# Kernel optimization log

Hardware: AMD Instinct MI355X
Metric: run time of the kernel (lower is better)

Reference implementation:

```python
import jax, jax.numpy as jnp
import numpy as np

H = 2  # num_heads hardcoded in the torch module


def setup_inputs() -> dict:
    key = jax.random.key(0)
    ks = jax.random.split(key, 10)
    B, S, D = 8, 2048, 512
    s = 0.02
    return {
        "rgb": jax.random.normal(ks[0], (B, S, D), jnp.float32),
        "event": jax.random.normal(ks[1], (B, S, D), jnp.float32),
        "w_rgb": jax.random.normal(ks[2], (D, D), jnp.float32) * s,
        "b_rgb": jnp.zeros((D,), jnp.float32),
        "w_event": jax.random.normal(ks[3], (D, D), jnp.float32) * s,
        "b_event": jnp.zeros((D,), jnp.float32),
        "w_in": jax.random.normal(ks[4], (3 * D, D), jnp.float32) * s,   # packed QKV in_proj, torch layout
        "b_in": jnp.zeros((3 * D,), jnp.float32),
        "w_out": jax.random.normal(ks[5], (D, D), jnp.float32) * s,
        "b_out": jnp.zeros((D,), jnp.float32),
    }


def _mha(q_in, kv_in, w_in, b_in, w_out, b_out):
    """torch nn.MultiheadAttention with key==value==kv_in, batch-first math."""
    B, S, D = q_in.shape
    hd = D // H
    q = q_in @ w_in[:D].T + b_in[:D]
    k = kv_in @ w_in[D:2 * D].T + b_in[D:2 * D]
    v = kv_in @ w_in[2 * D:].T + b_in[2 * D:]
    q = q.reshape(B, S, H, hd) * (1.0 / np.sqrt(hd))
    k = k.reshape(B, S, H, hd)
    v = v.reshape(B, S, H, hd)
    scores = jnp.einsum('bqhd,bkhd->bhqk', q, k)          # [B,H,S,S]
    attn = jax.nn.softmax(scores, axis=-1)
    out = jnp.einsum('bhqk,bkhd->bqhd', attn, v).reshape(B, S, D)
    return out @ w_out.T + b_out


def reference(rgb, event, w_rgb, b_rgb, w_event, b_event, w_in, b_in, w_out, b_out):
    rgb_p = rgb @ w_rgb.T + b_rgb
    event_p = event @ w_event.T + b_event
    # same attention weights used for both cross directions
    event_attn = _mha(rgb_p, event_p, w_in, b_in, w_out, b_out)
    rgb_attn = _mha(event_p, rgb_p, w_in, b_in, w_out, b_out)
    gate = jax.nn.sigmoid(jnp.sum(rgb_p * event_p, axis=-1, keepdims=True))
    fused = gate * event_attn + (1.0 - gate) * rgb_attn
    return fused + (rgb_p + event_p) * 0.5
```

## Files before the change

### kernel.cpp

```cpp
#include <hip/hip_runtime.h>
#include <hip/hip_bf16.h>
#include <stdint.h>


typedef __bf16 bf16_t;
typedef __bf16 bf16x8 __attribute__((ext_vector_type(8)));
typedef float f32x4 __attribute__((ext_vector_type(4)));
typedef float f32x16 __attribute__((ext_vector_type(16)));
typedef unsigned int u32;

typedef void gvoid_t __attribute__((address_space(1)));
typedef void svoid_t __attribute__((address_space(3)));

__device__ inline void gload16(const void* g, void* l) {
    __builtin_amdgcn_global_load_lds((gvoid_t*)g, (svoid_t*)l, 16, 0, 0);
}

__device__ inline u32 cvtpk_bf16(float lo, float hi) {
    u32 r;
    asm("v_cvt_pk_bf16_f32 %0, %1, %2" : "=v"(r) : "v"(lo), "v"(hi));
    return r;
}

__device__ inline float exp2v(float x) {
    float r;
    asm("v_exp_f32 %0, %1" : "=v"(r) : "v"(x));
    return r;
}

__global__ __launch_bounds__(256) void f2b_all(const float* __restrict__ s0, bf16_t* __restrict__ d0,
                                               const float* __restrict__ s1, bf16_t* __restrict__ d1,
                                               const float* __restrict__ s2, bf16_t* __restrict__ d2,
                                               const float* __restrict__ s3, bf16_t* __restrict__ d3,
                                               const float* __restrict__ s4, bf16_t* __restrict__ d4,
                                               const float* __restrict__ s5, bf16_t* __restrict__ d5) {
    int i = blockIdx.x * 256 + threadIdx.x;
    const float* s; bf16_t* d; int off;
    if (i < 1048576)      { s = s0; d = d0; off = i; }
    else if (i < 2097152) { s = s1; d = d1; off = i - 1048576; }
    else if (i < 2129920) { s = s2; d = d2; off = i - 2097152; }
    else if (i < 2162688) { s = s3; d = d3; off = i - 2129920; }
    else if (i < 2260992) { s = s4; d = d4; off = i - 2162688; }
    else                  { s = s5; d = d5; off = i - 2260992; }
    const float4* p = reinterpret_cast<const float4*>(s) + (size_t)off * 2;
    float4 a = p[0], b = p[1];
    bf16x8 o;
    o[0] = (bf16_t)a.x; o[1] = (bf16_t)a.y; o[2] = (bf16_t)a.z; o[3] = (bf16_t)a.w;
    o[4] = (bf16_t)b.x; o[5] = (bf16_t)b.y; o[6] = (bf16_t)b.z; o[7] = (bf16_t)b.w;
    reinterpret_cast<bf16x8*>(d)[off] = o;
}

template <int MODE>
__global__ __launch_bounds__(256) void gemm_bt(const bf16_t* __restrict__ A,
                                               const bf16_t* __restrict__ A2,
                                               const bf16_t* __restrict__ Bw,
                                               const bf16_t* __restrict__ Bw2,
                                               const float* __restrict__ bias,
                                               const float* __restrict__ bias2,
                                               void* __restrict__ Cout,
                                               void* __restrict__ Cout2,
                                               const bf16_t* __restrict__ r1,
                                               const bf16_t* __restrict__ r2,
                                               const float* __restrict__ gate,
                                               bf16_t* __restrict__ qdst,
                                               bf16_t* __restrict__ kdst,
                                               bf16_t* __restrict__ vdst,
                                               bf16_t* __restrict__ qdst2,
                                               bf16_t* __restrict__ kdst2,
                                               bf16_t* __restrict__ vdst2,
                                               int N, int K) {
    __shared__ __align__(16) bf16_t As[128][64];
    __shared__ __align__(16) bf16_t Bs[128][64];
    const int tid = threadIdx.x, lane = tid & 63, w = tid >> 6;
    const int l16 = lane & 15, l4 = lane >> 4;
    const int wm = w >> 1, wn = w & 1;
    const bool sec = (MODE != 2) && (blockIdx.y >= 128);
    const size_t a0 = (size_t)(blockIdx.y & 127) * 128;
    const size_t b0 = (size_t)blockIdx.x * 128;
    const bf16_t* Ap = sec ? A2 : A;
    const bf16_t* Bp = sec ? Bw2 : Bw;
    const float* bp = sec ? bias2 : bias;
    f32x4 acc[4][4] = {};
    const int srow = w * 32 + (lane >> 3);
    const int scol = (lane & 7) * 8;
    float g4[4];
    if (MODE == 2) {
#pragma unroll
        for (int i = 0; i < 4; ++i) g4[i] = gate[a0 + srow + i * 8];
    }
    for (int kt = 0; kt < K; kt += 64) {
        __syncthreads();
        if (MODE == 2) {
#pragma unroll
            for (int i = 0; i < 4; ++i) {
                size_t ro = (a0 + srow + i * 8) * (size_t)K + kt + scol;
                bf16x8 x = *reinterpret_cast<const bf16x8*>(A + ro);
                bf16x8 y = *reinterpret_cast<const bf16x8*>(A2 + ro);
                bf16x8 o;
#pragma unroll
                for (int j = 0; j < 8; ++j)
                    o[j] = (bf16_t)(g4[i] * (float)x[j] + (1.f - g4[i]) * (float)y[j]);
                *reinterpret_cast<bf16x8*>(&As[srow + i * 8 - (lane >> 3) + (lane >> 3)][scol]) = o;
            }
        } else {
#pragma unroll
            for (int i = 0; i < 4; ++i)
                gload16(Ap + (a0 + srow + i * 8) * (size_t)K + kt + scol, &As[w * 32 + i * 8][0]);
        }
#pragma unroll
        for (int i = 0; i < 4; ++i)
            gload16(Bp + (b0 + srow + i * 8) * (size_t)K + kt + scol, &Bs[w * 32 + i * 8][0]);
        __syncthreads();
#pragma unroll
        for (int kk = 0; kk < 2; ++kk) {
            bf16x8 af[4], bfr[4];
#pragma unroll
            for (int mi = 0; mi < 4; ++mi)
                af[mi] = *reinterpret_cast<const bf16x8*>(&As[wm * 64 + mi * 16 + l16][kk * 32 + l4 * 8]);
#pragma unroll
            for (int ni = 0; ni < 4; ++ni)
                bfr[ni] = *reinterpret_cast<const bf16x8*>(&Bs[wn * 64 + ni * 16 + l16][kk * 32 + l4 * 8]);
#pragma unroll
            for (int mi = 0; mi < 4; ++mi)
#pragma unroll
                for (int ni = 0; ni < 4; ++ni)
                    acc[mi][ni] = __builtin_amdgcn_mfma_f32_16x16x32_bf16(af[mi], bfr[ni], acc[mi][ni], 0, 0, 0);
        }
    }
    bf16_t* qd = sec ? qdst2 : qdst;
    bf16_t* kd = sec ? kdst2 : kdst;
    bf16_t* vd = sec ? vdst2 : vdst;
#pragma unroll
    for (int mi = 0; mi < 4; ++mi) {
#pragma unroll
        for (int ni = 0; ni < 4; ++ni) {
            int col = (int)b0 + wn * 64 + ni * 16 + l16;
            float bs = bp[col];
            int row0 = (int)a0 + wm * 64 + mi * 16 + l4 * 4;
            float vv[4];
#pragma unroll
            for (int r = 0; r < 4; ++r) vv[r] = acc[mi][ni][r] + bs;
            if (MODE == 0) {
                bf16_t* Cp = (bf16_t*)(sec ? Cout2 : Cout);
#pragma unroll
                for (int r = 0; r < 4; ++r)
                    Cp[(size_t)(row0 + r) * N + col] = (bf16_t)vv[r];
            } else if (MODE == 2) {
#pragma unroll
                for (int r = 0; r < 4; ++r) {
                    size_t idx = (size_t)(row0 + r) * N + col;
                    ((float*)Cout)[idx] = vv[r] + 0.5f * ((float)r1[idx] + (float)r2[idx]);
                }
            } else {
                if (col < 512) {
#pragma unroll
                    for (int r = 0; r < 4; ++r)
                        qd[(size_t)(row0 + r) * 512 + col] = (bf16_t)(vv[r] * 0.090168440f);
                } else if (col < 1024) {
                    int cc = col - 512, h = cc >> 8, d = cc & 255;
#pragma unroll
                    for (int r = 0; r < 4; ++r) {
                        int row = row0 + r;
                        int bh = (row >> 11) * 2 + h, seq = row & 2047;
                        kd[((size_t)(bh * 64 + (seq >> 5))) * 8192 + (d >> 3) * 256 +
                           (seq & 31) * 8 + (d & 7)] = (bf16_t)vv[r];
                    }
                } else {
                    int cc = col - 1024, h = cc >> 8, d = cc & 255;
                    int bh = (row0 >> 11) * 2 + h, seq = row0 & 2047;
                    size_t idx = ((size_t)(bh * 64 + (seq >> 5))) * 8192 +
                                 ((seq >> 3) & 3) * 2048 + d * 8 + (seq & 7);
                    union { bf16_t h4[4]; uint2 u8; } pk;
#pragma unroll
                    for (int r = 0; r < 4; ++r) pk.h4[r] = (bf16_t)vv[r];
                    *reinterpret_cast<uint2*>(&vd[idx]) = pk.u8;
                }
            }
        }
    }
}

__global__ __launch_bounds__(256) void gate_kernel(const bf16_t* __restrict__ rp,
                                                   const bf16_t* __restrict__ ep,
                                                   float* __restrict__ gate) {
    int row = blockIdx.x * 4 + (threadIdx.x >> 6);
    int lane = threadIdx.x & 63;
    bf16x8 a = reinterpret_cast<const bf16x8*>(rp + (size_t)row * 512)[lane];
    bf16x8 b = reinterpret_cast<const bf16x8*>(ep + (size_t)row * 512)[lane];
    float s = 0.f;
#pragma unroll
    for (int j = 0; j < 8; ++j) s += (float)a[j] * (float)b[j];
#pragma unroll
    for (int off = 32; off; off >>= 1) s += __shfl_xor(s, off, 64);
    if (lane == 0) gate[row] = 1.f / (1.f + __expf(-s));
}

__global__ __launch_bounds__(256, 2) void attn_kernel(const bf16_t* __restrict__ qbr,
                                                      const bf16_t* __restrict__ qbe,
                                                      const bf16_t* __restrict__ kbr,
                                                      const bf16_t* __restrict__ kbe,
                                                      const bf16_t* __restrict__ vbr,
                                                      const bf16_t* __restrict__ vbe,
                                                      bf16_t* __restrict__ out0,
                                                      bf16_t* __restrict__ out1) {
    __shared__ __align__(16) bf16_t smem[32768];
    const int bid = blockIdx.x;
    const int qb = bid >> 5;
    const int combo = bid & 31;
    const int dir = combo >> 4;
    const int bh = combo & 15;
    const int b = bh >> 1, h = bh & 1;
    const bf16_t* Qb = dir ? qbe : qbr;
    const bf16_t* Kc = dir ? kbr : kbe;
    const bf16_t* Vc = dir ? vbr : vbe;
    bf16_t* osrc = dir ? out1 : out0;
    const int tid = threadIdx.x;
    const int w = tid >> 6, l = tid & 63;
    const int l31 = l & 31, hi = l >> 5;
    const int q0w = qb * 128 + w * 32;

    const bf16_t* qp = Qb + ((size_t)(b * 2048 + q0w + l31)) * 512 + h * 256 + hi * 8;
    bf16x8 qf[16];
#pragma unroll
    for (int dch = 0; dch < 16; ++dch)
        qf[dch] = *reinterpret_cast<const bf16x8*>(qp + dch * 16);

    f32x16 O[8] = {};
    f32x16 st;
    float mrun = -1e30f, lrun = 0.f;
    union PA { u32 uw[4]; bf16x8 v; } pa0, pa1;

    const bf16_t* kq = Kc + (size_t)bh * 524288 + (w * 2048 + l * 8);
    const bf16_t* vq = Vc + (size_t)bh * 524288 + (w * 2048 + l * 8);

#define STAGE(T, P)                                                    \
    do {                                                               \
        const bf16_t* ks_ = kq + (size_t)(T) * 8192;                   \
        const bf16_t* vs_ = vq + (size_t)(T) * 8192;                   \
        bf16_t* lk_ = &smem[(P) * 8192 + w * 2048];                    \
        bf16_t* lv_ = &smem[16384 + (P) * 8192 + w * 2048];            \
        gload16(ks_, lk_); gload16(ks_ + 512, lk_ + 512);              \
        gload16(ks_ + 1024, lk_ + 1024); gload16(ks_ + 1536, lk_ + 1536); \
        gload16(vs_, lv_); gload16(vs_ + 512, lv_ + 512);              \
        gload16(vs_ + 1024, lv_ + 1024); gload16(vs_ + 1536, lv_ + 1536); \
    } while (0)

    STAGE(0, 0);

    for (int kt2 = 0; kt2 < 64; ++kt2) {
        asm volatile("s_waitcnt vmcnt(0)" ::: "memory");
        __builtin_amdgcn_s_barrier();
        if (kt2 < 63) STAGE(kt2 + 1, (kt2 + 1) & 1);

        const int cb = kt2 & 1;
        const bf16_t* kb = &smem[cb * 8192 + hi * 256 + l31 * 8];
        const bf16_t* vb = &smem[16384 + cb * 8192 + hi * 2048 + l31 * 8];

#pragma unroll
        for (int r = 0; r < 16; ++r) st[r] = 0.f;
        __builtin_amdgcn_s_setprio(1);
#pragma unroll
        for (int dch = 0; dch < 16; ++dch) {
            bf16x8 kf = *reinterpret_cast<const bf16x8*>(kb + dch * 512);
            st = __builtin_amdgcn_mfma_f32_32x32x16_bf16(kf, qf[dch], st, 0, 0, 0);
        }
        __builtin_amdgcn_s_setprio(0);

        float mx = st[0];
#pragma unroll
        for (int r = 1; r < 16; ++r) mx = fmaxf(mx, st[r]);
        mx = fmaxf(mx, __shfl_xor(mx, 32, 64));
        if (__any(mx - mrun > 8.f)) {
            float mnew = fmaxf(mrun, mx);
            float sc = exp2v(mrun - mnew);
            mrun = mnew;
            lrun *= sc;
#pragma unroll
            for (int r = 0; r < 16; ++r) {
                int qr = (r & 3) + 8 * (r >> 2) + 4 * hi;
                float scr = __shfl(sc, qr, 64);
#pragma unroll
                for (int g = 0; g < 8; ++g) O[g][r] *= scr;
            }
        }
        float lsum = 0.f;
        u32 W[8];
#pragma unroll
        for (int m = 0; m < 8; ++m) {
            float plo = exp2v(st[2 * m] - mrun);
            float phi_ = exp2v(st[2 * m + 1] - mrun);
            lsum += plo + phi_;
            W[m] = cvtpk_bf16(plo, phi_);
        }
        lsum += __shfl_xor(lsum, 32, 64);
        lrun += lsum;
        {
            u32 t0 = hi ? W[0] : W[2], t1 = hi ? W[1] : W[3];
            u32 r0 = (u32)__shfl_xor((int)t0, 32, 64);
            u32 r1 = (u32)__shfl_xor((int)t1, 32, 64);
            pa0.uw[0] = hi ? r0 : W[0]; pa0.uw[1] = hi ? r1 : W[1];
            pa0.uw[2] = hi ? W[2] : r0; pa0.uw[3] = hi ? W[3] : r1;
        }
        {
            u32 t0 = hi ? W[4] : W[6], t1 = hi ? W[5] : W[7];
            u32 r0 = (u32)__shfl_xor((int)t0, 32, 64);
            u32 r1 = (u32)__shfl_xor((int)t1, 32, 64);
            pa1.uw[0] = hi ? r0 : W[4]; pa1.uw[1] = hi ? r1 : W[5];
            pa1.uw[2] = hi ? W[6] : r0; pa1.uw[3] = hi ? W[7] : r1;
        }

        __builtin_amdgcn_s_setprio(1);
#pragma unroll
        for (int g = 0; g < 8; ++g) {
            bf16x8 v0 = *reinterpret_cast<const bf16x8*>(vb + g * 256);
            O[g] = __builtin_amdgcn_mfma_f32_32x32x16_bf16(pa0.v, v0, O[g], 0, 0, 0);
        }
#pragma unroll
        for (int g = 0; g < 8; ++g) {
            bf16x8 v1 = *reinterpret_cast<const bf16x8*>(vb + 4096 + g * 256);
            O[g] = __builtin_amdgcn_mfma_f32_32x32x16_bf16(pa1.v, v1, O[g], 0, 0, 0);
        }
        __builtin_amdgcn_s_setprio(0);
    }
#undef STAGE

#pragma unroll
    for (int r = 0; r < 16; ++r) {
        int qr = (r & 3) + 8 * (r >> 2) + 4 * hi;
        float linv = 1.0f / __shfl(lrun, qr, 64);
        size_t rowoff = ((size_t)(b * 2048 + q0w + qr)) * 512 + h * 256 + l31;
#pragma unroll
        for (int g = 0; g < 8; ++g)
            osrc[rowoff + g * 32] = (bf16_t)(O[g][r] * linv);
    }
}

extern "C" void kernel_launch(void* const* d_in, const int* in_sizes, int n_in,
                              void* d_out, int out_size, void* d_ws, size_t ws_size,
                              hipStream_t stream) {
    const float* rgb = (const float*)d_in[0];
    const float* event = (const float*)d_in[1];
    const float* w_rgb = (const float*)d_in[2];
    const float* b_rgb = (const float*)d_in[3];
    const float* w_event = (const float*)d_in[4];
    const float* b_event = (const float*)d_in[5];
    const float* w_in = (const float*)d_in[6];
    const float* b_in = (const float*)d_in[7];
    const float* w_out = (const float*)d_in[8];
    const float* b_out = (const float*)d_in[9];
    float* out = (float*)d_out;

    const size_t MB16 = (size_t)16 * 1024 * 1024;
    char* ws = (char*)d_ws;
    bf16_t* wrgb_bf = (bf16_t*)(ws + 0);
    bf16_t* wevt_bf = (bf16_t*)(ws + 524288);
    bf16_t* wout_bf = (bf16_t*)(ws + 1048576);
    bf16_t* win_bf = (bf16_t*)(ws + 1572864);
    float* gate = (float*)(ws + 3145728);
    bf16_t* bufA = (bf16_t*)(ws + 4194304);
    bf16_t* bufB = (bf16_t*)(ws + 4194304 + MB16);
    bf16_t* rgbp = (bf16_t*)(ws + 4194304 + 2 * MB16);
    bf16_t* evtp = (bf16_t*)(ws + 4194304 + 3 * MB16);
    bf16_t* qbr  = (bf16_t*)(ws + 4194304 + 4 * MB16);
    bf16_t* qbe  = (bf16_t*)(ws + 4194304 + 5 * MB16);
    bf16_t* kbr  = (bf16_t*)(ws + 4194304 + 6 * MB16);
    bf16_t* kbe  = (bf16_t*)(ws + 4194304 + 7 * MB16);
    bf16_t* vbr  = (bf16_t*)(ws + 4194304 + 8 * MB16);
    bf16_t* vbe  = (bf16_t*)(ws + 4194304 + 9 * MB16);

    dim3 blk(256);
    f2b_all<<<8960, blk, 0, stream>>>(rgb, bufA, event, bufB, w_rgb, wrgb_bf,
                                      w_event, wevt_bf, w_in, win_bf, w_out, wout_bf);
    gemm_bt<0><<<dim3(4, 256), blk, 0, stream>>>(bufA, bufB, wrgb_bf, wevt_bf, b_rgb, b_event,
                                                 rgbp, evtp, nullptr, nullptr, nullptr,
                                                 nullptr, nullptr, nullptr, nullptr, nullptr,
                                                 nullptr, 512, 512);
    gate_kernel<<<4096, blk, 0, stream>>>(rgbp, evtp, gate);
    gemm_bt<1><<<dim3(12, 256), blk, 0, stream>>>(rgbp, evtp, win_bf, win_bf, b_in, b_in,
                                                  nullptr, nullptr, nullptr, nullptr, nullptr,
                                                  qbr, kbr, vbr, qbe, kbe, vbe, 1536, 512);
    attn_kernel<<<512, blk, 0, stream>>>(qbr, qbe, kbr, kbe, vbr, vbe, bufA, bufB);
    gemm_bt<2><<<dim3(4, 128), blk, 0, stream>>>(bufA, bufB, wout_bf, nullptr, b_out, nullptr,
                                                 out, nullptr, rgbp, evtp, gate,
                                                 nullptr, nullptr, nullptr, nullptr, nullptr,
                                                 nullptr, 512, 512);
}
```

Measured before the change: 355.8 us.

## Store K row-major with XOR-swizzled LDS staging and split QK accumulators

Changes the K projection output layout from a tiled d-chunk layout to plain row-major per head, and loads K tiles into LDS with an XOR swizzle on the 16-byte column chunk, reading them back with the matching swizzle. This is meant to give coalesced writes from the projection epilogue and avoid LDS bank conflicts on K reads. It also splits the QK^T MFMA chain into two independent accumulators and tree-reduces the max and sum, shortening dependency chains at the cost of more registers.

```diff
diff --git a/kernel.cpp b/kernel.cpp
--- a/kernel.cpp
+++ b/kernel.cpp
@@ -100,7 +100,7 @@
 #pragma unroll
                 for (int j = 0; j < 8; ++j)
                     o[j] = (bf16_t)(g4[i] * (float)x[j] + (1.f - g4[i]) * (float)y[j]);
-                *reinterpret_cast<bf16x8*>(&As[srow + i * 8 - (lane >> 3) + (lane >> 3)][scol]) = o;
+                *reinterpret_cast<bf16x8*>(&As[srow + i * 8][scol]) = o;
             }
         } else {
 #pragma unroll
@@ -162,8 +162,7 @@
                     for (int r = 0; r < 4; ++r) {
                         int row = row0 + r;
                         int bh = (row >> 11) * 2 + h, seq = row & 2047;
-                        kd[((size_t)(bh * 64 + (seq >> 5))) * 8192 + (d >> 3) * 256 +
-                           (seq & 31) * 8 + (d & 7)] = (bf16_t)vv[r];
+                        kd[(size_t)bh * 524288 + (size_t)seq * 256 + d] = (bf16_t)vv[r];
                     }
                 } else {
                     int cc = col - 1024, h = cc >> 8, d = cc & 255;
@@ -226,23 +225,29 @@
         qf[dch] = *reinterpret_cast<const bf16x8*>(qp + dch * 16);
 
     f32x16 O[8] = {};
-    f32x16 st;
     float mrun = -1e30f, lrun = 0.f;
     union PA { u32 uw[4]; bf16x8 v; } pa0, pa1;
 
-    const bf16_t* kq = Kc + (size_t)bh * 524288 + (w * 2048 + l * 8);
+    const bf16_t* kq = Kc + (size_t)bh * 524288;
+    u32 koff[4];
+#pragma unroll
+    for (int i = 0; i < 4; ++i) {
+        int r = w * 8 + i * 2 + hi;
+        koff[i] = (u32)(r * 256 + ((l31 ^ r) * 8));
+    }
     const bf16_t* vq = Vc + (size_t)bh * 524288 + (w * 2048 + l * 8);
 
-#define STAGE(T, P)                                                    \
-    do {                                                               \
-        const bf16_t* ks_ = kq + (size_t)(T) * 8192;                   \
-        const bf16_t* vs_ = vq + (size_t)(T) * 8192;                   \
-        bf16_t* lk_ = &smem[(P) * 8192 + w * 2048];                    \
-        bf16_t* lv_ = &smem[16384 + (P) * 8192 + w * 2048];            \
-        gload16(ks_, lk_); gload16(ks_ + 512, lk_ + 512);              \
-        gload16(ks_ + 1024, lk_ + 1024); gload16(ks_ + 1536, lk_ + 1536); \
-        gload16(vs_, lv_); gload16(vs_ + 512, lv_ + 512);              \
-        gload16(vs_ + 1024, lv_ + 1024); gload16(vs_ + 1536, lv_ + 1536); \
+#define STAGE(T, P)                                                        \
+    do {                                                                   \
+        const bf16_t* kt_ = kq + (size_t)(T) * 8192;                       \
+        const bf16_t* vs_ = vq + (size_t)(T) * 8192;                       \
+        bf16_t* lv_ = &smem[16384 + (P) * 8192 + w * 2048];                \
+        gload16(kt_ + koff[0], &smem[(P) * 8192 + (w * 8 + 0) * 256]);     \
+        gload16(kt_ + koff[1], &smem[(P) * 8192 + (w * 8 + 2) * 256]);     \
+        gload16(kt_ + koff[2], &smem[(P) * 8192 + (w * 8 + 4) * 256]);     \
+        gload16(kt_ + koff[3], &smem[(P) * 8192 + (w * 8 + 6) * 256]);     \
+        gload16(vs_, lv_); gload16(vs_ + 512, lv_ + 512);                  \
+        gload16(vs_ + 1024, lv_ + 1024); gload16(vs_ + 1536, lv_ + 1536);  \
     } while (0)
 
     STAGE(0, 0);
@@ -253,22 +258,26 @@
         if (kt2 < 63) STAGE(kt2 + 1, (kt2 + 1) & 1);
 
         const int cb = kt2 & 1;
-        const bf16_t* kb = &smem[cb * 8192 + hi * 256 + l31 * 8];
+        const bf16_t* kb = &smem[cb * 8192 + l31 * 256];
         const bf16_t* vb = &smem[16384 + cb * 8192 + hi * 2048 + l31 * 8];
 
-#pragma unroll
-        for (int r = 0; r < 16; ++r) st[r] = 0.f;
+        f32x16 st0 = {}, st1 = {};
         __builtin_amdgcn_s_setprio(1);
 #pragma unroll
-        for (int dch = 0; dch < 16; ++dch) {
-            bf16x8 kf = *reinterpret_cast<const bf16x8*>(kb + dch * 512);
-            st = __builtin_amdgcn_mfma_f32_32x32x16_bf16(kf, qf[dch], st, 0, 0, 0);
+        for (int dp = 0; dp < 8; ++dp) {
+            bf16x8 k0 = *reinterpret_cast<const bf16x8*>(kb + (((2 * dp) * 2 + hi) ^ l31) * 8);
+            st0 = __builtin_amdgcn_mfma_f32_32x32x16_bf16(k0, qf[2 * dp], st0, 0, 0, 0);
+            bf16x8 k1 = *reinterpret_cast<const bf16x8*>(kb + (((2 * dp + 1) * 2 + hi) ^ l31) * 8);
+            st1 = __builtin_amdgcn_mfma_f32_32x32x16_bf16(k1, qf[2 * dp + 1], st1, 0, 0, 0);
         }
         __builtin_amdgcn_s_setprio(0);
-
-        float mx = st[0];
-#pragma unroll
-        for (int r = 1; r < 16; ++r) mx = fmaxf(mx, st[r]);
+        f32x16 st = st0 + st1;
+
+        float mx4[4];
+#pragma unroll
+        for (int j = 0; j < 4; ++j)
+            mx4[j] = fmaxf(fmaxf(st[4 * j], st[4 * j + 1]), fmaxf(st[4 * j + 2], st[4 * j + 3]));
+        float mx = fmaxf(fmaxf(mx4[0], mx4[1]), fmaxf(mx4[2], mx4[3]));
         mx = fmaxf(mx, __shfl_xor(mx, 32, 64));
         if (__any(mx - mrun > 8.f)) {
             float mnew = fmaxf(mrun, mx);
@@ -283,15 +292,17 @@
                 for (int g = 0; g < 8; ++g) O[g][r] *= scr;
             }
         }
-        float lsum = 0.f;
+        float p_[16];
+#pragma unroll
+        for (int r = 0; r < 16; ++r) p_[r] = exp2v(st[r] - mrun);
         u32 W[8];
 #pragma unroll
-        for (int m = 0; m < 8; ++m) {
-            float plo = exp2v(st[2 * m] - mrun);
-            float phi_ = exp2v(st[2 * m + 1] - mrun);
-            lsum += plo + phi_;
-            W[m] = cvtpk_bf16(plo, phi_);
-        }
+        for (int m = 0; m < 8; ++m) W[m] = cvtpk_bf16(p_[2 * m], p_[2 * m + 1]);
+        float s4[4];
+#pragma unroll
+        for (int j = 0; j < 4; ++j)
+            s4[j] = (p_[4 * j] + p_[4 * j + 1]) + (p_[4 * j + 2] + p_[4 * j + 3]);
+        float lsum = (s4[0] + s4[1]) + (s4[2] + s4[3]);
         lsum += __shfl_xor(lsum, 32, 64);
         lrun += lsum;
         {
```

After: 358.1 us. No clear change (+0.6%).

## Process two 32-row query tiles per wave in attention to reuse K/V fragments

Applied to the files above, without the earlier changes.

Each wave of the attention kernel now handles 64 query rows (two 32-row sub-tiles) instead of 32. Every K and V fragment read from LDS feeds two MFMAs, which halves LDS traffic and global K/V staging per query row. The grid shrinks from 512 to 256 blocks and launch bounds drop to one block per CU. The cost is a much larger register footprint (two Q fragment sets and two O accumulators), lower occupancy, and only 256 blocks for 256 CUs, so latency hiding and load balance may suffer.

```diff
diff --git a/kernel.cpp b/kernel.cpp
--- a/kernel.cpp
+++ b/kernel.cpp
@@ -100,7 +100,7 @@
 #pragma unroll
                 for (int j = 0; j < 8; ++j)
                     o[j] = (bf16_t)(g4[i] * (float)x[j] + (1.f - g4[i]) * (float)y[j]);
-                *reinterpret_cast<bf16x8*>(&As[srow + i * 8 - (lane >> 3) + (lane >> 3)][scol]) = o;
+                *reinterpret_cast<bf16x8*>(&As[srow + i * 8][scol]) = o;
             }
         } else {
 #pragma unroll
@@ -195,7 +195,7 @@
     if (lane == 0) gate[row] = 1.f / (1.f + __expf(-s));
 }
 
-__global__ __launch_bounds__(256, 2) void attn_kernel(const bf16_t* __restrict__ qbr,
+__global__ __launch_bounds__(256, 1) void attn_kernel(const bf16_t* __restrict__ qbr,
                                                       const bf16_t* __restrict__ qbe,
                                                       const bf16_t* __restrict__ kbr,
                                                       const bf16_t* __restrict__ kbe,
@@ -217,18 +217,20 @@
     const int tid = threadIdx.x;
     const int w = tid >> 6, l = tid & 63;
     const int l31 = l & 31, hi = l >> 5;
-    const int q0w = qb * 128 + w * 32;
-
-    const bf16_t* qp = Qb + ((size_t)(b * 2048 + q0w + l31)) * 512 + h * 256 + hi * 8;
-    bf16x8 qf[16];
-#pragma unroll
-    for (int dch = 0; dch < 16; ++dch)
-        qf[dch] = *reinterpret_cast<const bf16x8*>(qp + dch * 16);
-
-    f32x16 O[8] = {};
-    f32x16 st;
-    float mrun = -1e30f, lrun = 0.f;
-    union PA { u32 uw[4]; bf16x8 v; } pa0, pa1;
+    const int q0w = qb * 256 + w * 64;
+
+    const bf16_t* qp0 = Qb + ((size_t)(b * 2048 + q0w + l31)) * 512 + h * 256 + hi * 8;
+    const bf16_t* qp1 = qp0 + 32 * 512;
+    bf16x8 qf0[16], qf1[16];
+#pragma unroll
+    for (int dch = 0; dch < 16; ++dch) {
+        qf0[dch] = *reinterpret_cast<const bf16x8*>(qp0 + dch * 16);
+        qf1[dch] = *reinterpret_cast<const bf16x8*>(qp1 + dch * 16);
+    }
+
+    f32x16 O0[8] = {}, O1[8] = {};
+    float mrun0 = -1e30f, lrun0 = 0.f, mrun1 = -1e30f, lrun1 = 0.f;
+    union PA { u32 uw[4]; bf16x8 v; } pa00, pa01, pa10, pa11;
 
     const bf16_t* kq = Kc + (size_t)bh * 524288 + (w * 2048 + l * 8);
     const bf16_t* vq = Vc + (size_t)bh * 524288 + (w * 2048 + l * 8);
@@ -245,6 +247,49 @@
         gload16(vs_ + 1024, lv_ + 1024); gload16(vs_ + 1536, lv_ + 1536); \
     } while (0)
 
+#define SOFTMAX(STP, MRUN, LRUN, PA0, PA1, OA)                                \
+    do {                                                                      \
+        float mx_ = STP[0];                                                   \
+        _Pragma("unroll") for (int r_ = 1; r_ < 16; ++r_)                     \
+            mx_ = fmaxf(mx_, STP[r_]);                                        \
+        mx_ = fmaxf(mx_, __shfl_xor(mx_, 32, 64));                            \
+        if (__any(mx_ - MRUN > 8.f)) {                                        \
+            float mnew_ = fmaxf(MRUN, mx_);                                   \
+            float sc_ = exp2v(MRUN - mnew_);                                  \
+            MRUN = mnew_; LRUN *= sc_;                                        \
+            _Pragma("unroll") for (int r_ = 0; r_ < 16; ++r_) {               \
+                int qr_ = (r_ & 3) + 8 * (r_ >> 2) + 4 * hi;                  \
+                float scr_ = __shfl(sc_, qr_, 64);                            \
+                _Pragma("unroll") for (int g_ = 0; g_ < 8; ++g_)              \
+                    OA[g_][r_] *= scr_;                                       \
+            }                                                                 \
+        }                                                                     \
+        float ls_ = 0.f;                                                      \
+        u32 W_[8];                                                            \
+        _Pragma("unroll") for (int m_ = 0; m_ < 8; ++m_) {                    \
+            float plo_ = exp2v(STP[2 * m_] - MRUN);                           \
+            float phi_ = exp2v(STP[2 * m_ + 1] - MRUN);                       \
+            ls_ += plo_ + phi_;                                               \
+            W_[m_] = cvtpk_bf16(plo_, phi_);                                  \
+        }                                                                     \
+        ls_ += __shfl_xor(ls_, 32, 64);                                       \
+        LRUN += ls_;                                                          \
+        {                                                                     \
+            u32 t0_ = hi ? W_[0] : W_[2], t1_ = hi ? W_[1] : W_[3];           \
+            u32 r0_ = (u32)__shfl_xor((int)t0_, 32, 64);                      \
+            u32 r1_ = (u32)__shfl_xor((int)t1_, 32, 64);                      \
+            PA0.uw[0] = hi ? r0_ : W_[0]; PA0.uw[1] = hi ? r1_ : W_[1];       \
+            PA0.uw[2] = hi ? W_[2] : r0_; PA0.uw[3] = hi ? W_[3] : r1_;       \
+        }                                                                     \
+        {                                                                     \
+            u32 t0_ = hi ? W_[4] : W_[6], t1_ = hi ? W_[5] : W_[7];           \
+            u32 r0_ = (u32)__shfl_xor((int)t0_, 32, 64);                      \
+            u32 r1_ = (u32)__shfl_xor((int)t1_, 32, 64);                      \
+            PA1.uw[0] = hi ? r0_ : W_[4]; PA1.uw[1] = hi ? r1_ : W_[5];       \
+            PA1.uw[2] = hi ? W_[6] : r0_; PA1.uw[3] = hi ? W_[7] : r1_;       \
+        }                                                                     \
+    } while (0)
+
     STAGE(0, 0);
 
     for (int kt2 = 0; kt2 < 64; ++kt2) {
@@ -256,82 +301,49 @@
         const bf16_t* kb = &smem[cb * 8192 + hi * 256 + l31 * 8];
         const bf16_t* vb = &smem[16384 + cb * 8192 + hi * 2048 + l31 * 8];
 
-#pragma unroll
-        for (int r = 0; r < 16; ++r) st[r] = 0.f;
+        f32x16 st0 = {}, st1 = {};
         __builtin_amdgcn_s_setprio(1);
 #pragma unroll
         for (int dch = 0; dch < 16; ++dch) {
             bf16x8 kf = *reinterpret_cast<const bf16x8*>(kb + dch * 512);
-            st = __builtin_amdgcn_mfma_f32_32x32x16_bf16(kf, qf[dch], st, 0, 0, 0);
+            st0 = __builtin_amdgcn_mfma_f32_32x32x16_bf16(kf, qf0[dch], st0, 0, 0, 0);
+            st1 = __builtin_amdgcn_mfma_f32_32x32x16_bf16(kf, qf1[dch], st1, 0, 0, 0);
         }
         __builtin_amdgcn_s_setprio(0);
 
-        float mx = st[0];
-#pragma unroll
-        for (int r = 1; r < 16; ++r) mx = fmaxf(mx, st[r]);
-        mx = fmaxf(mx, __shfl_xor(mx, 32, 64));
-        if (__any(mx - mrun > 8.f)) {
-            float mnew = fmaxf(mrun, mx);
-            float sc = exp2v(mrun - mnew);
-            mrun = mnew;
-            lrun *= sc;
-#pragma unroll
-            for (int r = 0; r < 16; ++r) {
-                int qr = (r & 3) + 8 * (r >> 2) + 4 * hi;
-                float scr = __shfl(sc, qr, 64);
-#pragma unroll
-                for (int g = 0; g < 8; ++g) O[g][r] *= scr;
-            }
-        }
-        float lsum = 0.f;
-        u32 W[8];
-#pragma unroll
-        for (int m = 0; m < 8; ++m) {
-            float plo = exp2v(st[2 * m] - mrun);
-            float phi_ = exp2v(st[2 * m + 1] - mrun);
-            lsum += plo + phi_;
-            W[m] = cvtpk_bf16(plo, phi_);
-        }
-        lsum += __shfl_xor(lsum, 32, 64);
-        lrun += lsum;
-        {
-            u32 t0 = hi ? W[0] : W[2], t1 = hi ? W[1] : W[3];
-            u32 r0 = (u32)__shfl_xor((int)t0, 32, 64);
-            u32 r1 = (u32)__shfl_xor((int)t1, 32, 64);
-            pa0.uw[0] = hi ? r0 : W[0]; pa0.uw[1] = hi ? r1 : W[1];
-            pa0.uw[2] = hi ? W[2] : r0; pa0.uw[3] = hi ? W[3] : r1;
-        }
-        {
-            u32 t0 = hi ? W[4] : W[6], t1 = hi ? W[5] : W[7];
-            u32 r0 = (u32)__shfl_xor((int)t0, 32, 64);
-            u32 r1 = (u32)__shfl_xor((int)t1, 32, 64);
-            pa1.uw[0] = hi ? r0 : W[4]; pa1.uw[1] = hi ? r1 : W[5];
-            pa1.uw[2] = hi ? W[6] : r0; pa1.uw[3] = hi ? W[7] : r1;
-        }
+        SOFTMAX(st0, mrun0, lrun0, pa00, pa01, O0);
+        SOFTMAX(st1, mrun1, lrun1, pa10, pa11, O1);
 
         __builtin_amdgcn_s_setprio(1);
 #pragma unroll
         for (int g = 0; g < 8; ++g) {
             bf16x8 v0 = *reinterpret_cast<const bf16x8*>(vb + g * 256);
-            O[g] = __builtin_amdgcn_mfma_f32_32x32x16_bf16(pa0.v, v0, O[g], 0, 0, 0);
+            O0[g] = __builtin_amdgcn_mfma_f32_32x32x16_bf16(pa00.v, v0, O0[g], 0, 0, 0);
+            O1[g] = __builtin_amdgcn_mfma_f32_32x32x16_bf16(pa10.v, v0, O1[g], 0, 0, 0);
         }
 #pragma unroll
         for (int g = 0; g < 8; ++g) {
             bf16x8 v1 = *reinterpret_cast<const bf16x8*>(vb + 4096 + g * 256);
-            O[g] = __builtin_amdgcn_mfma_f32_32x32x16_bf16(pa1.v, v1, O[g], 0, 0, 0);
+            O0[g] = __builtin_amdgcn_mfma_f32_32x32x16_bf16(pa01.v, v1, O0[g], 0, 0, 0);
+            O1[g] = __builtin_amdgcn_mfma_f32_32x32x16_bf16(pa11.v, v1, O1[g], 0, 0, 0);
         }
         __builtin_amdgcn_s_setprio(0);
     }
 #undef STAGE
+#undef SOFTMAX
 
 #pragma unroll
     for (int r = 0; r < 16; ++r) {
         int qr = (r & 3) + 8 * (r >> 2) + 4 * hi;
-        float linv = 1.0f / __shfl(lrun, qr, 64);
-        size_t rowoff = ((size_t)(b * 2048 + q0w + qr)) * 512 + h * 256 + l31;
-#pragma unroll
-        for (int g = 0; g < 8; ++g)
-            osrc[rowoff + g * 32] = (bf16_t)(O[g][r] * linv);
+        float linv0 = 1.0f / __shfl(lrun0, qr, 64);
+        float linv1 = 1.0f / __shfl(lrun1, qr, 64);
+        size_t row0 = ((size_t)(b * 2048 + q0w + qr)) * 512 + h * 256 + l31;
+        size_t row1 = row0 + (size_t)32 * 512;
+#pragma unroll
+        for (int g = 0; g < 8; ++g) {
+            osrc[row0 + g * 32] = (bf16_t)(O0[g][r] * linv0);
+            osrc[row1 + g * 32] = (bf16_t)(O1[g][r] * linv1);
+        }
     }
 }
 
@@ -379,7 +391,7 @@
     gemm_bt<1><<<dim3(12, 256), blk, 0, stream>>>(rgbp, evtp, win_bf, win_bf, b_in, b_in,
                                                   nullptr, nullptr, nullptr, nullptr, nullptr,
                                                   qbr, kbr, vbr, qbe, kbe, vbe, 1536, 512);
-    attn_kernel<<<512, blk, 0, stream>>>(qbr, qbe, kbr, kbe, vbr, vbe, bufA, bufB);
+    attn_kernel<<<256, blk, 0, stream>>>(qbr, qbe, kbr, kbe, vbr, vbe, bufA, bufB);
     gemm_bt<2><<<dim3(4, 128), blk, 0, stream>>>(bufA, bufB, wout_bf, nullptr, b_out, nullptr,
                                                  out, nullptr, rgbp, evtp, gate,
                                                  nullptr, nullptr, nullptr, nullptr, nullptr,
```

Measured after the change: 1.223 ms. +243.8%, slower.
